# Kernel optimization log

Hardware: AMD Instinct MI355X
Metric: run time of the kernel (lower is better)

## Reference

```python
import jax, jax.numpy as jnp
import numpy as np

H = 16      # num_heads
DH = 64     # dim_heads


def rotate_half(x):
    # '... (j d) -> ... j d', j=2; unbind -> (x1, x2); cat(-x2, x1)
    x1, x2 = jnp.split(x, 2, axis=-1)
    return jnp.concatenate([-x2, x1], axis=-1)


def apply_rope(t, freqs):
    # t: [b, h, s, d], freqs: [s, d] (rot_dim == d, so no unrotated tail)
    return t * jnp.cos(freqs) + rotate_half(t) * jnp.sin(freqs)


def setup_inputs() -> dict:
    key = jax.random.key(0)
    k1, k2, k3, k4 = jax.random.split(key, 4)
    B, S, D = 2, 2048, 1024
    x = jax.random.normal(k1, (B, S, D), dtype=jnp.float32)
    w_qkv = jax.random.normal(k2, (D, 3 * D), dtype=jnp.float32) * (D ** -0.5)
    w_out = jax.random.normal(k3, (D, D), dtype=jnp.float32) * (D ** -0.5)
    freqs = jax.random.normal(k4, (S, DH), dtype=jnp.float32)
    return {"x": x, "w_qkv": w_qkv, "w_out": w_out, "freqs": freqs}


def reference(x, w_qkv, w_out, freqs):
    B, S, D = x.shape
    qkv = x @ w_qkv                                   # [B, S, 3D]
    q, k, v = jnp.split(qkv, 3, axis=-1)
    def to_heads(t):
        return t.reshape(B, S, H, DH).transpose(0, 2, 1, 3)  # [B, H, S, DH]
    q, k, v = map(to_heads, (q, k, v))
    # rotary (computed in float32, which is already the working dtype)
    q = apply_rope(q, freqs)
    k = apply_rope(k, freqs)
    # causal SDPA, scale = 1/sqrt(dh)
    scale = DH ** -0.5
    scores = jnp.einsum('bhqd,bhkd->bhqk', q, k) * scale
    causal_mask = jnp.tril(jnp.ones((S, S), dtype=bool))
    scores = jnp.where(causal_mask, scores, jnp.finfo(scores.dtype).min)
    attn = jax.nn.softmax(scores, axis=-1)
    out = jnp.einsum('bhqk,bhkd->bhqd', attn, v)      # [B, H, S, DH]
    out = out.transpose(0, 2, 1, 3).reshape(B, S, D)  # 'b h n d -> b n (h d)'
    return out @ w_out
```

## Files before the change

kernel.cpp:

```cpp
#include <hip/hip_runtime.h>


typedef __bf16 bf16x8 __attribute__((ext_vector_type(8)));
typedef float f32x4 __attribute__((ext_vector_type(4)));

__device__ __forceinline__ unsigned short f2b(float f) {
  unsigned int u = __builtin_bit_cast(unsigned int, f);
  unsigned int lsb = (u >> 16) & 1u;
  u += 0x7fffu + lsb;
  return (unsigned short)(u >> 16);
}
__device__ __forceinline__ float b2f(unsigned short h) {
  unsigned int u = ((unsigned int)h) << 16;
  return __builtin_bit_cast(float, u);
}
__device__ __forceinline__ unsigned int pk2(float a, float b) {
  return (unsigned int)f2b(a) | ((unsigned int)f2b(b) << 16);
}
__device__ __forceinline__ unsigned int cvtpk(float lo, float hi) {
  unsigned int r;
  asm("v_cvt_pk_bf16_f32 %0, %1, %2" : "=v"(r) : "v"(lo), "v"(hi));
  return r;
}
__device__ __forceinline__ void gload16(const void* g, void* l) {
  __builtin_amdgcn_global_load_lds(
      (const __attribute__((address_space(1))) unsigned int*)g,
      (__attribute__((address_space(3))) unsigned int*)l, 16, 0, 0);
}

__global__ __launch_bounds__(256) void prologue_kernel(
    const float* __restrict__ x, unsigned short* __restrict__ xb,
    const float* __restrict__ freqs, float* __restrict__ cosT,
    float* __restrict__ sinT, const float* __restrict__ w_qkv,
    unsigned short* __restrict__ wqT, const float* __restrict__ w_out,
    unsigned short* __restrict__ woT) {
  __shared__ float tile[32][33];
  const int blk = blockIdx.x, tid = threadIdx.x;

  if (blk < 4096) {
    int i = (blk * 256 + tid) * 4;
    float4 v = *(const float4*)&x[i];
    ushort4 o;
    o.x = f2b(v.x); o.y = f2b(v.y); o.z = f2b(v.z); o.w = f2b(v.w);
    *(ushort4*)&xb[i] = o;
    return;
  }
  if (blk < 4608) {
    int i = (blk - 4096) * 256 + tid;
    float f = freqs[i];
    cosT[i] = cosf(f);
    sinT[i] = sinf(f);
    return;
  }
  const float* src;
  unsigned short* dst;
  int K, N, bx, by;
  if (blk < 7680) {
    src = w_qkv; dst = wqT; K = 1024; N = 3072;
    const int t = blk - 4608;
    bx = t % 96; by = t / 96;
  } else {
    src = w_out; dst = woT; K = 1024; N = 1024;
    const int t = blk - 7680;
    bx = t % 32; by = t / 32;
  }
  const int n0 = bx * 32, k0 = by * 32;
  const int c = tid & 31, r4 = tid >> 5;
#pragma unroll
  for (int p = 0; p < 4; ++p) {
    int r = r4 + p * 8;
    tile[r][c] = src[(size_t)(k0 + r) * N + n0 + c];
  }
  __syncthreads();
#pragma unroll
  for (int p = 0; p < 4; ++p) {
    int r = r4 + p * 8;
    dst[(size_t)(n0 + r) * K + k0 + c] = f2b(tile[c][r]);
  }
}

__global__ __launch_bounds__(256, 3) void gemm_fused(
    const unsigned short* __restrict__ A, const unsigned short* __restrict__ BT,
    unsigned short* __restrict__ Qb, unsigned short* __restrict__ Kbp,
    unsigned short* __restrict__ Vtg, const float* __restrict__ cosT,
    const float* __restrict__ sinT) {
  extern __shared__ unsigned short L[];
  const int K = 1024;
  const int tid = threadIdx.x, lane = tid & 63, w = tid >> 6;
  const int wr = w >> 1, wc = w & 1;
  const int fr = lane & 15, oct = lane >> 4;

  const int m0 = blockIdx.y * 128, n0 = blockIdx.x * 128;

  const int sr = tid >> 2;
  const int scol = ((tid & 3) ^ ((tid >> 3) & 3)) * 8;
  const size_t aR0 = (size_t)(m0 + sr) * K + scol;
  const size_t aR1 = (size_t)(m0 + 64 + sr) * K + scol;
  const size_t bR0 = (size_t)(n0 + sr) * K + scol;
  const size_t bR1 = (size_t)(n0 + 64 + sr) * K + scol;

  f32x4 acc[4][4] = {};
  const int T = K >> 5;

  for (int pt = 0; pt < 2; ++pt) {
    unsigned short* Ln = &L[pt * 8192];
    const size_t gk = (size_t)pt * 32;
    gload16(&A[aR0 + gk], &Ln[tid * 8]);
    gload16(&A[aR1 + gk], &Ln[2048 + tid * 8]);
    gload16(&BT[bR0 + gk], &Ln[4096 + tid * 8]);
    gload16(&BT[bR1 + gk], &Ln[6144 + tid * 8]);
  }

  int cs = 0;
  for (int t = 0; t < T; ++t) {
    if (t + 2 <= T) {
      asm volatile("s_waitcnt vmcnt(4)" ::: "memory");
    } else {
      asm volatile("s_waitcnt vmcnt(0)" ::: "memory");
    }
    __builtin_amdgcn_sched_barrier(0);
    __builtin_amdgcn_s_barrier();
    __builtin_amdgcn_sched_barrier(0);

    const unsigned short* Lb = &L[cs * 8192];
    const int sslot = (cs == 0) ? 2 : cs - 1;
    unsigned short* Ln = &L[sslot * 8192];
    const size_t gk = (size_t)(t + 2) * 32;
    const bool doStage = (t + 2 < T);

    bf16x8 af[4], bq[4];
#pragma unroll
    for (int i = 0; i < 4; ++i) {
      const int ra = wr * 64 + i * 16 + fr;
      af[i] = __builtin_bit_cast(
          bf16x8, *(const uint4*)&Lb[ra * 32 + ((oct ^ ((ra >> 1) & 3)) * 8)]);
    }
#pragma unroll
    for (int j = 0; j < 4; ++j) {
      const int rb = wc * 64 + j * 16 + fr;
      bq[j] = __builtin_bit_cast(
          bf16x8,
          *(const uint4*)&Lb[4096 + rb * 32 + ((oct ^ ((rb >> 1) & 3)) * 8)]);
    }
    if (doStage) {
      gload16(&A[aR0 + gk], &Ln[tid * 8]);
      gload16(&A[aR1 + gk], &Ln[2048 + tid * 8]);
      gload16(&BT[bR0 + gk], &Ln[4096 + tid * 8]);
      gload16(&BT[bR1 + gk], &Ln[6144 + tid * 8]);
    }
    __builtin_amdgcn_s_setprio(1);
#pragma unroll
    for (int i = 0; i < 4; ++i)
#pragma unroll
      for (int j = 0; j < 4; ++j)
        acc[i][j] = __builtin_amdgcn_mfma_f32_16x16x32_bf16(af[i], bq[j], acc[i][j], 0, 0, 0);
    __builtin_amdgcn_s_setprio(0);

    cs = (cs == 2) ? 0 : cs + 1;
  }

  const float QSCALE = 0.125f * 1.44269504f;
  const int part = n0 >> 10;
  const int hh = ((n0 & 1023) >> 6) + wc;
  if (part < 2) {
    unsigned short* dst = (part == 0) ? Qb : Kbp;
    const float scale = (part == 0) ? QSCALE : 1.0f;
#pragma unroll
    for (int i = 0; i < 4; ++i)
#pragma unroll
      for (int r = 0; r < 4; ++r) {
        const int m = m0 + wr * 64 + i * 16 + oct * 4 + r;
        const int bb = m >> 11, s = m & 2047;
        const size_t ob = ((size_t)(bb * 16 + hh) * 2048 + s) * 64;
#pragma unroll
        for (int j = 0; j < 2; ++j) {
          const int d = j * 16 + fr;
          const float lo = acc[i][j][r], hi = acc[i][j + 2][r];
          const float cl = cosT[s * 64 + d], sl = sinT[s * 64 + d];
          const float ch = cosT[s * 64 + 32 + d], sh = sinT[s * 64 + 32 + d];
          dst[ob + d] = f2b((lo * cl - hi * sl) * scale);
          dst[ob + 32 + d] = f2b((hi * ch + lo * sh) * scale);
        }
      }
  } else {
    __syncthreads();
    unsigned short* vt = L + (w)*4224;
#pragma unroll
    for (int i = 0; i < 4; ++i)
#pragma unroll
      for (int r = 0; r < 4; ++r) {
        const int s64 = i * 16 + oct * 4 + r;
#pragma unroll
        for (int j = 0; j < 4; ++j) vt[s64 * 66 + j * 16 + fr] = f2b(acc[i][j][r]);
      }
    __syncthreads();
    const int tix = tid >> 6, d = tid & 63;
    const int wrt = tix >> 1, wct = tix & 1;
    const unsigned short* tt = L + tix * 4224;
    const int mtile = m0 + wrt * 64;
    const int bb = mtile >> 11, sb = (mtile & 2047) >> 6;
    const int hv = ((n0 & 1023) >> 6) + wct;
    const size_t vb = (((size_t)(bb * 16 + hv) * 32 + sb) * 64 + d) * 64;
#pragma unroll
    for (int qq = 0; qq < 4; ++qq)
#pragma unroll
      for (int g = 0; g < 4; ++g) {
        ushort4 u;
        u.x = tt[(qq * 16 + g * 4 + 0) * 66 + d];
        u.y = tt[(qq * 16 + g * 4 + 1) * 66 + d];
        u.z = tt[(qq * 16 + g * 4 + 2) * 66 + d];
        u.w = tt[(qq * 16 + g * 4 + 3) * 66 + d];
        *(ushort4*)&Vtg[vb + (qq >> 1) * 32 + g * 8 + (qq & 1) * 4] = u;
      }
  }
}

__global__ __launch_bounds__(256, 2) void gemm2_ring(const unsigned short* __restrict__ A,
                                                     const unsigned short* __restrict__ BT,
                                                     float* __restrict__ C,
                                                     int M, int N, int K) {
  extern __shared__ unsigned short L[];
  const int tid = threadIdx.x, lane = tid & 63, w = tid >> 6;
  const int wr = w >> 1, wc = w & 1;
  const int fr = lane & 15, oct = lane >> 4;
  const int m0 = blockIdx.y * 128, n0 = blockIdx.x * 64;

  const int sr = tid >> 2;
  const int scol = ((tid & 3) ^ ((tid >> 3) & 3)) * 8;
  const size_t aR0 = (size_t)(m0 + sr) * K + scol;
  const size_t aR1 = (size_t)(m0 + 64 + sr) * K + scol;
  const size_t bR0 = (size_t)(n0 + sr) * K + scol;

  f32x4 acc[4][2] = {};
  const int T = K >> 5;

  for (int pt = 0; pt < 3; ++pt) {
    unsigned short* Ln = &L[pt * 6144];
    const size_t gk = (size_t)pt * 32;
    gload16(&A[aR0 + gk], &Ln[tid * 8]);
    gload16(&A[aR1 + gk], &Ln[2048 + tid * 8]);
    gload16(&BT[bR0 + gk], &Ln[4096 + tid * 8]);
  }

  for (int t = 0; t < T; ++t) {
    if (t + 3 <= T) {
      asm volatile("s_waitcnt vmcnt(6)" ::: "memory");
    } else if (t + 2 == T) {
      asm volatile("s_waitcnt vmcnt(3)" ::: "memory");
    } else {
      asm volatile("s_waitcnt vmcnt(0)" ::: "memory");
    }
    __builtin_amdgcn_sched_barrier(0);
    __builtin_amdgcn_s_barrier();
    __builtin_amdgcn_sched_barrier(0);

    const unsigned short* Lb = &L[(t & 3) * 6144];
    unsigned short* Ln = &L[((t + 3) & 3) * 6144];
    const size_t gk = (size_t)(t + 3) * 32;
    const bool doStage = (t + 3 < T);

    bf16x8 af[4], bq[2];
#pragma unroll
    for (int i = 0; i < 4; ++i) {
      const int ra = wr * 64 + i * 16 + fr;
      af[i] = __builtin_bit_cast(
          bf16x8, *(const uint4*)&Lb[ra * 32 + ((oct ^ ((ra >> 1) & 3)) * 8)]);
    }
#pragma unroll
    for (int j = 0; j < 2; ++j) {
      const int rb = wc * 32 + j * 16 + fr;
      bq[j] = __builtin_bit_cast(
          bf16x8,
          *(const uint4*)&Lb[4096 + rb * 32 + ((oct ^ ((rb >> 1) & 3)) * 8)]);
    }
    if (doStage) {
      gload16(&A[aR0 + gk], &Ln[tid * 8]);
      gload16(&A[aR1 + gk], &Ln[2048 + tid * 8]);
      gload16(&BT[bR0 + gk], &Ln[4096 + tid * 8]);
    }
    __builtin_amdgcn_s_setprio(1);
#pragma unroll
    for (int i = 0; i < 4; ++i)
#pragma unroll
      for (int j = 0; j < 2; ++j)
        acc[i][j] = __builtin_amdgcn_mfma_f32_16x16x32_bf16(af[i], bq[j], acc[i][j], 0, 0, 0);
    __builtin_amdgcn_s_setprio(0);
  }

#pragma unroll
  for (int i = 0; i < 4; ++i)
#pragma unroll
    for (int j = 0; j < 2; ++j)
#pragma unroll
      for (int r = 0; r < 4; ++r)
        C[(size_t)(m0 + wr * 64 + i * 16 + oct * 4 + r) * N + n0 + wc * 32 +
          j * 16 + fr] = acc[i][j][r];
}

__global__ __launch_bounds__(512, 4) void attn_mfma(const unsigned short* __restrict__ Qb,
                                                    const unsigned short* __restrict__ Kb,
                                                    const unsigned short* __restrict__ Vtg,
                                                    unsigned short* __restrict__ attnb) {
  extern __shared__ unsigned short KV[];
  const int bid = blockIdx.x + 16 * (blockIdx.y + 16 * blockIdx.z);
  const int xcd = bid & 7, slot = bid >> 3;
  const int qt0 = slot & 15;
  const int gq = xcd + 8 * (slot >> 4);
  const int h = gq & 15, b = gq >> 4;
  const int qt1 = 31 - qt0;
  const int tid = threadIdx.x, lane = tid & 63, w = tid >> 6;
  const int fr = lane & 15, oct = lane >> 4;
  const int grp = w >> 2, wq = w & 3;
  const int nhA = 16 - qt0, nhB = 15 - qt0;

  const size_t bh = (size_t)(b * 16 + h);
  const unsigned short* Kbase = Kb + bh * 131072;
  const unsigned short* Vbase = Vtg + bh * 131072;

  const int qtP1 = grp ? qt1 : qt0;
  const unsigned short* Qp1 = Qb + (bh * 2048 + qtP1 * 64 + wq * 16 + fr) * 64;
  const bf16x8 qa0 = __builtin_bit_cast(bf16x8, *(const uint4*)(Qp1 + oct * 8));
  const bf16x8 qa1 = __builtin_bit_cast(bf16x8, *(const uint4*)(Qp1 + 32 + oct * 8));
  const unsigned short* Qp2 = Qb + (bh * 2048 + qt1 * 64 + wq * 16 + fr) * 64;
  const bf16x8 qb0 = __builtin_bit_cast(bf16x8, *(const uint4*)(Qp2 + oct * 8));
  const bf16x8 qb1 = __builtin_bit_cast(bf16x8, *(const uint4*)(Qp2 + 32 + oct * 8));

  const int frx = fr & 7;
  const int rc0 = (oct ^ frx) * 8;
  const int rc1 = ((4 + oct) ^ frx) * 8;

  float m_prev = -1e30f;
  f32x4 acc[4] = {};
  f32x4 accl = {};

  uint4 onesu;
  onesu.x = 0x3F803F80u; onesu.y = 0x3F803F80u;
  onesu.z = 0x3F803F80u; onesu.w = 0x3F803F80u;
  const bf16x8 onesf = __builtin_bit_cast(bf16x8, onesu);

  auto tile_step = [&](int buf, bf16x8 q0, bf16x8 q1, bool domask) {
    const unsigned short* Kbuf = &KV[buf * 4096];
    const unsigned short* Vbuf = &KV[(4 + buf) * 4096];
    f32x4 s4[4];
    __builtin_amdgcn_s_setprio(1);
#pragma unroll
    for (int t = 0; t < 4; ++t) {
      bf16x8 kf0 = __builtin_bit_cast(bf16x8, *(const uint4*)&Kbuf[(t * 16 + fr) * 64 + rc0]);
      bf16x8 kf1 = __builtin_bit_cast(bf16x8, *(const uint4*)&Kbuf[(t * 16 + fr) * 64 + rc1]);
      f32x4 s = {};
      s = __builtin_amdgcn_mfma_f32_16x16x32_bf16(kf0, q0, s, 0, 0, 0);
      s = __builtin_amdgcn_mfma_f32_16x16x32_bf16(kf1, q1, s, 0, 0, 0);
      s4[t] = s;
    }
    __builtin_amdgcn_s_setprio(0);
    if (domask) {
#pragma unroll
      for (int t = 0; t < 4; ++t)
#pragma unroll
        for (int r = 0; r < 4; ++r)
          if (t * 16 + oct * 4 + r > wq * 16 + fr) s4[t][r] = -1e30f;
    }

    float pm = -1e30f;
#pragma unroll
    for (int t = 0; t < 4; ++t)
#pragma unroll
      for (int r = 0; r < 4; ++r) pm = fmaxf(pm, s4[t][r]);
    const bool need = __any(pm - m_prev > 11.0f);
    if (need) {
      float pmf = fmaxf(pm, __shfl_xor(pm, 16));
      pmf = fmaxf(pmf, __shfl_xor(pmf, 32));
      float mnew = fmaxf(m_prev, pmf);
      float cf = __builtin_amdgcn_exp2f(m_prev - mnew);
      m_prev = mnew;
      float cfr[4];
#pragma unroll
      for (int r = 0; r < 4; ++r) cfr[r] = __shfl(cf, oct * 4 + r);
#pragma unroll
      for (int t2 = 0; t2 < 4; ++t2)
#pragma unroll
        for (int r = 0; r < 4; ++r) acc[t2][r] *= cfr[r];
#pragma unroll
      for (int r = 0; r < 4; ++r) accl[r] *= cfr[r];
    }
    const float mc = m_prev;
#pragma unroll
    for (int t = 0; t < 4; ++t)
#pragma unroll
      for (int r = 0; r < 4; ++r)
        s4[t][r] = __builtin_amdgcn_exp2f(s4[t][r] - mc);

    uint4 pw0, pw1;
    pw0.x = cvtpk(s4[0][0], s4[0][1]); pw0.y = cvtpk(s4[0][2], s4[0][3]);
    pw0.z = cvtpk(s4[1][0], s4[1][1]); pw0.w = cvtpk(s4[1][2], s4[1][3]);
    pw1.x = cvtpk(s4[2][0], s4[2][1]); pw1.y = cvtpk(s4[2][2], s4[2][3]);
    pw1.z = cvtpk(s4[3][0], s4[3][1]); pw1.w = cvtpk(s4[3][2], s4[3][3]);
    const bf16x8 pa0 = __builtin_bit_cast(bf16x8, pw0);
    const bf16x8 pa1 = __builtin_bit_cast(bf16x8, pw1);

    __builtin_amdgcn_s_setprio(1);
#pragma unroll
    for (int t2 = 0; t2 < 4; ++t2) {
      bf16x8 vf0 = __builtin_bit_cast(bf16x8, *(const uint4*)&Vbuf[(t2 * 16 + fr) * 64 + rc0]);
      bf16x8 vf1 = __builtin_bit_cast(bf16x8, *(const uint4*)&Vbuf[(t2 * 16 + fr) * 64 + rc1]);
      f32x4 a = acc[t2];
      a = __builtin_amdgcn_mfma_f32_16x16x32_bf16(pa0, vf0, a, 0, 0, 0);
      a = __builtin_amdgcn_mfma_f32_16x16x32_bf16(pa1, vf1, a, 0, 0, 0);
      acc[t2] = a;
    }
    {
      f32x4 a = accl;
      a = __builtin_amdgcn_mfma_f32_16x16x32_bf16(pa0, onesf, a, 0, 0, 0);
      a = __builtin_amdgcn_mfma_f32_16x16x32_bf16(pa1, onesf, a, 0, 0, 0);
      accl = a;
    }
    __builtin_amdgcn_s_setprio(0);
  };

  auto write_out = [&](int qtile) {
#pragma unroll
    for (int r = 0; r < 4; ++r) {
      float linv = 1.f / accl[r];
      size_t orow = (size_t)(b * 2048 + qtile * 64 + wq * 16 + oct * 4 + r);
#pragma unroll
      for (int t2 = 0; t2 < 4; ++t2)
        attnb[orow * 1024 + h * 64 + t2 * 16 + fr] = f2b(acc[t2][r] * linv);
    }
  };

  const int srow = tid >> 3, lc1 = tid & 7;
  const int soff = srow * 64 + (lc1 ^ (srow & 7)) * 8;
  const unsigned short* kp1 = Kbase + srow * 64 + lc1 * 8;
  const unsigned short* vp1 = Vbase + srow * 64 + lc1 * 8;
  {
    uint4 kr = *(const uint4*)kp1;
    uint4 vr = *(const uint4*)vp1;
    *(uint4*)&KV[0 * 4096 + soff] = kr;
    *(uint4*)&KV[4 * 4096 + soff] = vr;
  }
  __syncthreads();

  for (int kb = 0; kb <= qt0; ++kb) {
    uint4 kr = *(const uint4*)(kp1 + (size_t)(kb + 1) * 4096);
    uint4 vr = *(const uint4*)(vp1 + (size_t)(kb + 1) * 4096);
    uint4 kr2, vr2;
    const bool extra = (kb == qt0) && (nhB > 0);
    if (extra) {
      kr2 = *(const uint4*)(kp1 + (size_t)17 * 4096);
      vr2 = *(const uint4*)(vp1 + (size_t)17 * 4096);
    }
    tile_step(kb & 1, qa0, qa1, kb == qtP1);
    const int nb = (kb + 1) & 1;
    *(uint4*)&KV[nb * 4096 + soff] = kr;
    *(uint4*)&KV[(4 + nb) * 4096 + soff] = vr;
    if (extra) {
      *(uint4*)&KV[2 * 4096 + soff] = kr2;
      *(uint4*)&KV[6 * 4096 + soff] = vr2;
    }
    __syncthreads();
  }

  if (grp == 0) {
    write_out(qt0);
    m_prev = -1e30f;
    f32x4 zz = {};
    accl = zz;
#pragma unroll
    for (int t2 = 0; t2 < 4; ++t2) acc[t2] = zz;
  }

  const int t2id = tid & 255;
  const int sk2 = t2id >> 2, lq = t2id & 3;
  const int lcA = lq * 2, lcB = lq * 2 + 1;
  const int ofA = sk2 * 64 + (lcA ^ (sk2 & 7)) * 8;
  const int ofB = sk2 * 64 + (lcB ^ (sk2 & 7)) * 8;
  const int sc2 = lq * 16;
  const int cnt = grp ? nhB : nhA;
  for (int i = 0; i < nhA; ++i) {
    const int kbm = grp ? (17 + i) : (qt0 + 1 + i);
    const int buf = grp ? (2 + (i & 1)) : (kbm & 1);
    uint4 k0, k1, v0, v1;
    const bool pf = (i + 1 < cnt);
    if (pf) {
      const unsigned short* ks = Kbase + (size_t)((kbm + 1) * 64 + sk2) * 64 + sc2;
      const unsigned short* vs = Vbase + (size_t)((kbm + 1) * 64 + sk2) * 64 + sc2;
      k0 = *(const uint4*)ks; k1 = *(const uint4*)(ks + 8);
      v0 = *(const uint4*)vs; v1 = *(const uint4*)(vs + 8);
    }
    if (i < cnt) tile_step(buf, qb0, qb1, kbm == qt1);
    if (pf) {
      const int nb = grp ? (2 + ((i + 1) & 1)) : ((kbm + 1) & 1);
      *(uint4*)&KV[nb * 4096 + ofA] = k0;
      *(uint4*)&KV[nb * 4096 + ofB] = k1;
      *(uint4*)&KV[(4 + nb) * 4096 + ofA] = v0;
      *(uint4*)&KV[(4 + nb) * 4096 + ofB] = v1;
    }
    __syncthreads();
  }

  float* MF = (float*)KV;
  if (grp == 1) {
#pragma unroll
    for (int t2 = 0; t2 < 4; ++t2)
#pragma unroll
      for (int r = 0; r < 4; ++r)
        MF[(wq * 16 + oct * 4 + r) * 68 + t2 * 16 + fr] = acc[t2][r];
    if (fr == 0) {
#pragma unroll
      for (int r = 0; r < 4; ++r) MF[4352 + wq * 16 + oct * 4 + r] = accl[r];
    }
    if (oct == 0) MF[4416 + wq * 16 + fr] = m_prev;
  }
  __syncthreads();
  if (grp == 0) {
    float mB = MF[4416 + wq * 16 + fr];
    float mS = fmaxf(m_prev, mB);
    float fA = __builtin_amdgcn_exp2f(m_prev - mS);
    float fB = __builtin_amdgcn_exp2f(mB - mS);
    float fAr[4], fBr[4];
#pragma unroll
    for (int r = 0; r < 4; ++r) {
      fAr[r] = __shfl(fA, oct * 4 + r);
      fBr[r] = __shfl(fB, oct * 4 + r);
    }
#pragma unroll
    for (int r = 0; r < 4; ++r)
      accl[r] = accl[r] * fAr[r] + MF[4352 + wq * 16 + oct * 4 + r] * fBr[r];
#pragma unroll
    for (int t2 = 0; t2 < 4; ++t2)
#pragma unroll
      for (int r = 0; r < 4; ++r)
        acc[t2][r] = acc[t2][r] * fAr[r] +
                     MF[(wq * 16 + oct * 4 + r) * 68 + t2 * 16 + fr] * fBr[r];
    write_out(qt1);
  }
}

extern "C" void kernel_launch(void* const* d_in, const int* in_sizes, int n_in,
                              void* d_out, int out_size, void* d_ws, size_t ws_size,
                              hipStream_t stream) {
  const float* x     = (const float*)d_in[0];
  const float* w_qkv = (const float*)d_in[1];
  const float* w_out = (const float*)d_in[2];
  const float* freqs = (const float*)d_in[3];
  float* out = (float*)d_out;

  char* ws = (char*)d_ws;
  unsigned short* Qb   = (unsigned short*)(ws + 25165824);
  unsigned short* Kb   = (unsigned short*)(ws + 33554432);
  unsigned short* Vtg  = (unsigned short*)(ws + 41943040);
  unsigned short* attnb= (unsigned short*)(ws + 50331648);
  unsigned short* wqT  = (unsigned short*)(ws + 58720256);
  unsigned short* woT  = (unsigned short*)(ws + 65011712);
  unsigned short* xb   = (unsigned short*)(ws + 67108864);
  float* cosT          = (float*)(ws + 75497472);
  float* sinT          = (float*)(ws + 76021760);

  (void)hipFuncSetAttribute((const void*)gemm_fused,
                            hipFuncAttributeMaxDynamicSharedMemorySize, 49152);
  (void)hipFuncSetAttribute((const void*)gemm2_ring,
                            hipFuncAttributeMaxDynamicSharedMemorySize, 49152);
  (void)hipFuncSetAttribute((const void*)attn_mfma,
                            hipFuncAttributeMaxDynamicSharedMemorySize, 65536);

  prologue_kernel<<<8704, 256, 0, stream>>>(x, xb, freqs, cosT, sinT, w_qkv,
                                            wqT, w_out, woT);
  gemm_fused<<<dim3(24, 32), 256, 49152, stream>>>(xb, wqT, Qb, Kb, Vtg, cosT,
                                                   sinT);
  attn_mfma<<<dim3(16, 16, 2), 512, 65536, stream>>>(Qb, Kb, Vtg, attnb);
  gemm2_ring<<<dim3(16, 32), 256, 49152, stream>>>(attnb, woT, out, 4096, 1024, 1024);
}
```

Measured before the change: 93.05 us.

## Use 512 threads per block in QKV GEMM, halving per-wave tile rows

The fused QKV GEMM now launches 8 waves per block instead of 4, with each wave computing a 32x64 sub-tile instead of 64x64. Global-to-LDS staging is split across twice as many threads, so each thread issues two loads instead of four, and the wait count is adjusted to match. The V transpose epilogue is remapped so two waves share each 64x64 staging tile. This cuts accumulator registers per wave and adds more waves to hide latency, at the cost of lower per-wave MFMA reuse of the B fragments and more LDS reads per FLOP.

```diff
diff --git a/kernel.cpp b/kernel.cpp
--- a/kernel.cpp
+++ b/kernel.cpp
@@ -79,7 +79,7 @@
   }
 }
 
-__global__ __launch_bounds__(256, 3) void gemm_fused(
+__global__ __launch_bounds__(512, 6) void gemm_fused(
     const unsigned short* __restrict__ A, const unsigned short* __restrict__ BT,
     unsigned short* __restrict__ Qb, unsigned short* __restrict__ Kbp,
     unsigned short* __restrict__ Vtg, const float* __restrict__ cosT,
@@ -92,29 +92,24 @@
 
   const int m0 = blockIdx.y * 128, n0 = blockIdx.x * 128;
 
-  const int sr = tid >> 2;
   const int scol = ((tid & 3) ^ ((tid >> 3) & 3)) * 8;
-  const size_t aR0 = (size_t)(m0 + sr) * K + scol;
-  const size_t aR1 = (size_t)(m0 + 64 + sr) * K + scol;
-  const size_t bR0 = (size_t)(n0 + sr) * K + scol;
-  const size_t bR1 = (size_t)(n0 + 64 + sr) * K + scol;
-
-  f32x4 acc[4][4] = {};
+  const size_t aR = (size_t)(m0 + (tid >> 2)) * K + scol;
+  const size_t bR = (size_t)(n0 + (tid >> 2)) * K + scol;
+
+  f32x4 acc[2][4] = {};
   const int T = K >> 5;
 
   for (int pt = 0; pt < 2; ++pt) {
     unsigned short* Ln = &L[pt * 8192];
     const size_t gk = (size_t)pt * 32;
-    gload16(&A[aR0 + gk], &Ln[tid * 8]);
-    gload16(&A[aR1 + gk], &Ln[2048 + tid * 8]);
-    gload16(&BT[bR0 + gk], &Ln[4096 + tid * 8]);
-    gload16(&BT[bR1 + gk], &Ln[6144 + tid * 8]);
+    gload16(&A[aR + gk], &Ln[tid * 8]);
+    gload16(&BT[bR + gk], &Ln[4096 + tid * 8]);
   }
 
   int cs = 0;
   for (int t = 0; t < T; ++t) {
     if (t + 2 <= T) {
-      asm volatile("s_waitcnt vmcnt(4)" ::: "memory");
+      asm volatile("s_waitcnt vmcnt(2)" ::: "memory");
     } else {
       asm volatile("s_waitcnt vmcnt(0)" ::: "memory");
     }
@@ -128,10 +123,10 @@
     const size_t gk = (size_t)(t + 2) * 32;
     const bool doStage = (t + 2 < T);
 
-    bf16x8 af[4], bq[4];
-#pragma unroll
-    for (int i = 0; i < 4; ++i) {
-      const int ra = wr * 64 + i * 16 + fr;
+    bf16x8 af[2], bq[4];
+#pragma unroll
+    for (int i = 0; i < 2; ++i) {
+      const int ra = wr * 32 + i * 16 + fr;
       af[i] = __builtin_bit_cast(
           bf16x8, *(const uint4*)&Lb[ra * 32 + ((oct ^ ((ra >> 1) & 3)) * 8)]);
     }
@@ -143,14 +138,12 @@
           *(const uint4*)&Lb[4096 + rb * 32 + ((oct ^ ((rb >> 1) & 3)) * 8)]);
     }
     if (doStage) {
-      gload16(&A[aR0 + gk], &Ln[tid * 8]);
-      gload16(&A[aR1 + gk], &Ln[2048 + tid * 8]);
-      gload16(&BT[bR0 + gk], &Ln[4096 + tid * 8]);
-      gload16(&BT[bR1 + gk], &Ln[6144 + tid * 8]);
+      gload16(&A[aR + gk], &Ln[tid * 8]);
+      gload16(&BT[bR + gk], &Ln[4096 + tid * 8]);
     }
     __builtin_amdgcn_s_setprio(1);
 #pragma unroll
-    for (int i = 0; i < 4; ++i)
+    for (int i = 0; i < 2; ++i)
 #pragma unroll
       for (int j = 0; j < 4; ++j)
         acc[i][j] = __builtin_amdgcn_mfma_f32_16x16x32_bf16(af[i], bq[j], acc[i][j], 0, 0, 0);
@@ -166,10 +159,10 @@
     unsigned short* dst = (part == 0) ? Qb : Kbp;
     const float scale = (part == 0) ? QSCALE : 1.0f;
 #pragma unroll
-    for (int i = 0; i < 4; ++i)
+    for (int i = 0; i < 2; ++i)
 #pragma unroll
       for (int r = 0; r < 4; ++r) {
-        const int m = m0 + wr * 64 + i * 16 + oct * 4 + r;
+        const int m = m0 + wr * 32 + i * 16 + oct * 4 + r;
         const int bb = m >> 11, s = m & 2047;
         const size_t ob = ((size_t)(bb * 16 + hh) * 2048 + s) * 64;
 #pragma unroll
@@ -184,25 +177,26 @@
       }
   } else {
     __syncthreads();
-    unsigned short* vt = L + (w)*4224;
-#pragma unroll
-    for (int i = 0; i < 4; ++i)
+    unsigned short* vt = L + ((wr >> 1) * 2 + wc) * 4224;
+#pragma unroll
+    for (int i = 0; i < 2; ++i)
 #pragma unroll
       for (int r = 0; r < 4; ++r) {
-        const int s64 = i * 16 + oct * 4 + r;
+        const int s64 = (wr & 1) * 32 + i * 16 + oct * 4 + r;
 #pragma unroll
         for (int j = 0; j < 4; ++j) vt[s64 * 66 + j * 16 + fr] = f2b(acc[i][j][r]);
       }
     __syncthreads();
-    const int tix = tid >> 6, d = tid & 63;
-    const int wrt = tix >> 1, wct = tix & 1;
-    const unsigned short* tt = L + tix * 4224;
-    const int mtile = m0 + wrt * 64;
+    const int tix2 = tid >> 6, d = tid & 63;
+    const int tile = tix2 >> 1, qh = tix2 & 1;
+    const unsigned short* tt = L + tile * 4224;
+    const int mtile = m0 + (tile >> 1) * 64;
     const int bb = mtile >> 11, sb = (mtile & 2047) >> 6;
-    const int hv = ((n0 & 1023) >> 6) + wct;
+    const int hv = ((n0 & 1023) >> 6) + (tile & 1);
     const size_t vb = (((size_t)(bb * 16 + hv) * 32 + sb) * 64 + d) * 64;
 #pragma unroll
-    for (int qq = 0; qq < 4; ++qq)
+    for (int q2 = 0; q2 < 2; ++q2) {
+      const int qq = qh * 2 + q2;
 #pragma unroll
       for (int g = 0; g < 4; ++g) {
         ushort4 u;
@@ -212,6 +206,7 @@
         u.w = tt[(qq * 16 + g * 4 + 3) * 66 + d];
         *(ushort4*)&Vtg[vb + (qq >> 1) * 32 + g * 8 + (qq & 1) * 4] = u;
       }
+    }
   }
 }
 
@@ -565,7 +560,7 @@
 
   prologue_kernel<<<8704, 256, 0, stream>>>(x, xb, freqs, cosT, sinT, w_qkv,
                                             wqT, w_out, woT);
-  gemm_fused<<<dim3(24, 32), 256, 49152, stream>>>(xb, wqT, Qb, Kb, Vtg, cosT,
+  gemm_fused<<<dim3(24, 32), 512, 49152, stream>>>(xb, wqT, Qb, Kb, Vtg, cosT,
                                                    sinT);
   attn_mfma<<<dim3(16, 16, 2), 512, 65536, stream>>>(Qb, Kb, Vtg, attnb);
   gemm2_ring<<<dim3(16, 32), 256, 49152, stream>>>(attnb, woT, out, 4096, 1024, 1024);
```

Result: no change. 93.18 us (+0.1%).
